# Kernel optimization log

Hardware: AMD Instinct MI355X
Metric: run time of the kernel (lower is better)

The kernel has to match this reference:

```python
import jax, jax.numpy as jnp
import numpy as np

NF = 64      # feature channels of h
K = 3        # dynamic filter spatial size (padding=1 in source implies k=3)
FACTOR = 4   # pixel-unshuffle factor


def shuffle_down(x, f):
    # torch pixel_unshuffle: (B,C,H*f,W*f) -> (B,C*f*f,H,W)
    B, C, H, W = x.shape
    x = x.reshape(B, C, H // f, f, W // f, f)
    x = x.transpose(0, 1, 3, 5, 2, 4)
    return x.reshape(B, C * f * f, H // f, W // f)


def _patches3x3(x):
    # x: (B,C,H,W) -> (B,C,9,H,W): zero-padded 3x3 neighborhoods, row-major taps,
    # identical to the identity-filter grouped conv (im2col) in the source.
    H, W = x.shape[-2], x.shape[-1]
    xp = jnp.pad(x, ((0, 0), (0, 0), (1, 1), (1, 1)))
    shifts = [xp[:, :, dy:dy + H, dx:dx + W] for dy in range(K) for dx in range(K)]
    return jnp.stack(shifts, axis=2)


def setup_inputs() -> dict:
    key = jax.random.key(0)
    k1, k2, k3, k4 = jax.random.split(key, 4)
    B, H, W = 2, 256, 256
    h = jax.random.normal(k1, (B, NF, H, W), dtype=jnp.float32)
    i_t = jax.random.normal(k2, (B, 3, H * FACTOR, W * FACTOR), dtype=jnp.float32)
    conv_w = jax.random.normal(k3, (K * K, 3 * FACTOR ** 2, K, K), dtype=jnp.float32) * 0.05
    conv_b = jax.random.normal(k4, (K * K,), dtype=jnp.float32) * 0.05
    return {"h": h, "i_t": i_t, "conv_w": conv_w, "conv_b": conv_b}


def reference(h, i_t, conv_w, conv_b):
    # predict per-pixel 3x3 filters from the shuffled-down guidance frame
    x = shuffle_down(i_t, FACTOR)  # (B, 48, H, W)
    f = jax.lax.conv_general_dilated(
        x, conv_w, window_strides=(1, 1), padding=((1, 1), (1, 1)),
        dimension_numbers=("NCHW", "OIHW", "NCHW"))
    filters = jax.nn.relu(f + conv_b[None, :, None, None])  # (B, 9, H, W)

    # dynamic per-pixel conv: same 3x3 filter applied to every channel of h
    patches = _patches3x3(h)  # (B, nf, 9, H, W)
    out = jnp.einsum("bcfhw,bfhw->bchw", patches, filters)  # (B, nf, H, W)
    return out
```

## Files before the change

### kernel.cpp

```cpp
#include <hip/hip_runtime.h>

#define HSZ 256
#define WSZ 256
#define NFC 64
#define PLANE (HSZ * WSZ)

typedef __attribute__((ext_vector_type(8))) short short8;
typedef __attribute__((ext_vector_type(4))) float f32x4;

__device__ inline unsigned short f2bf(float f) {
    unsigned u = __builtin_bit_cast(unsigned, f);
    return (unsigned short)((u + 0x7fffu + ((u >> 16) & 1u)) >> 16);
}

__global__ __launch_bounds__(256, 4) void fused_dynfilter_v4(
    const float* __restrict__ hbuf,
    const float* __restrict__ i_t,
    const float* __restrict__ wbuf,
    const float* __restrict__ bias,
    float* __restrict__ out)
{
    __shared__ __align__(16) unsigned char smem[32688];
    unsigned short* const xs  = (unsigned short*)smem;
    unsigned short* const lwT = (unsigned short*)(smem + 20160);
    float* const lf = (float*)(smem + 28080);

    const int tid = threadIdx.x;

    const int lin = blockIdx.x + 16 * (blockIdx.y + 32 * blockIdx.z);
    const int q   = ((int)gridDim.z * 512) >> 3;
    const int nid = (lin & 7) * q + (lin >> 3);
    const int b   = nid >> 9;
    const int rem = nid & 511;
    const int X0  = (rem & 15) * 16;
    const int Y0  = (rem >> 4) * 8;

    const int lane = tid & 63;
    const int l15  = lane & 15;
    const int kg   = lane >> 4;
    const int wv   = tid >> 6;

    const float bv = (l15 < 9) ? bias[l15] : 0.f;
    const float* itb = i_t + (size_t)b * 3 * (PLANE * 16);

    {
        float4 lreg[9]; int sdst[9];
#pragma unroll
        for (int k = 0; k < 9; ++k) {
            const int v = tid + 256 * k;
            const int sp = v / 12, t = v - sp * 12;
            const int c3 = t >> 2, fy = t & 3;
            const int ly = sp / 18, lx = sp - ly * 18;
            const int Y = Y0 - 1 + ly, X = X0 - 1 + lx;
            float4 val = make_float4(0.f, 0.f, 0.f, 0.f);
            if (v < 2160 && (unsigned)Y < HSZ && (unsigned)X < WSZ)
                val = *(const float4*)(itb + ((size_t)c3 * 1024 + (4 * Y + fy)) * 1024 + 4 * X);
            lreg[k] = val;
            sdst[k] = (v < 2160) ? (sp * 56 + t * 4) : -1;
        }
#pragma unroll
        for (int k = 0; k < 9; ++k)
            if (sdst[k] >= 0) {
                ushort4 u{f2bf(lreg[k].x), f2bf(lreg[k].y), f2bf(lreg[k].z), f2bf(lreg[k].w)};
                *(ushort4*)(xs + sdst[k]) = u;
            }
    }

    {
        float4 wr[4];
#pragma unroll
        for (int k = 0; k < 4; ++k) {
            const int v = tid + 256 * k;
            wr[k] = (v < 972) ? *(const float4*)(wbuf + (size_t)v * 4)
                              : make_float4(0.f, 0.f, 0.f, 0.f);
        }
#pragma unroll
        for (int k = 0; k < 4; ++k) {
            const int v = tid + 256 * k;
            if (v < 972) {
                const float e[4] = {wr[k].x, wr[k].y, wr[k].z, wr[k].w};
#pragma unroll
                for (int j = 0; j < 4; ++j) {
                    const int n  = v * 4 + j;
                    const int oc = n / 432;
                    const int r  = n - 432 * oc;
                    const int ic = r / 9;
                    const int kk = r - 9 * ic;
                    lwT[oc * 440 + kk * 48 + ic] = f2bf(e[j]);
                }
            }
        }
    }

    __syncthreads();

    short8 wf[14];
    {
        const unsigned short* lwb = lwT + l15 * 440 + kg * 8;
#pragma unroll
        for (int kb = 0; kb < 14; ++kb) {
            short8 w = {0, 0, 0, 0, 0, 0, 0, 0};
            if (l15 < 9 && !(kb == 13 && kg >= 2))
                w = *(const short8*)(lwb + kb * 32);
            wf[kb] = w;
        }
    }

    f32x4 acc0 = {0.f, 0.f, 0.f, 0.f}, acc1 = acc0;
#pragma unroll
    for (int kb = 0; kb < 14; ++kb) {
        const int k0 = kb * 32 + kg * 8;
        int off = 0;
        if (k0 < 432) {
            const int kk = k0 / 48, ic0 = k0 - 48 * kk;
            const int ky = kk / 3, kx = kk - 3 * ky;
            off = ((2 * wv + ky) * 18 + l15 + kx) * 56 + ic0;
        }
        short8 a0 = *(const short8*)(xs + off);
        short8 a1 = *(const short8*)(xs + off + 1008);
        acc0 = __builtin_amdgcn_mfma_f32_16x16x32_bf16(a0, wf[kb], acc0, 0, 0, 0);
        acc1 = __builtin_amdgcn_mfma_f32_16x16x32_bf16(a1, wf[kb], acc1, 0, 0, 0);
    }

    if (l15 < 9) {
#pragma unroll
        for (int t = 0; t < 2; ++t) {
            const int py = 2 * wv + t;
            const f32x4 A = t ? acc1 : acc0;
#pragma unroll
            for (int r = 0; r < 4; ++r)
                lf[l15 * 128 + py * 16 + (kg * 4 + r)] = fmaxf(A[r] + bv, 0.f);
        }
    }

    __syncthreads();

    const int pq  = tid & 3;
    const int pyA = (tid >> 2) & 7;
    const int clo = tid >> 5;

    float4 flt[9];
#pragma unroll
    for (int oc = 0; oc < 9; ++oc)
        flt[oc] = *(const float4*)(lf + oc * 128 + pyA * 16 + pq * 4);

    const int col0 = X0 + pq * 4;
    const int Yc   = Y0 + pyA;
    const bool gl  = (col0 > 0);
    const bool gr  = (col0 < WSZ - 4);

    bool rg[3]; int roff[3];
#pragma unroll
    for (int ky = 0; ky < 3; ++ky) {
        const int Y = Yc - 1 + ky;
        rg[ky]   = ((unsigned)Y < HSZ);
        roff[ky] = Y * WSZ + col0;
    }

    const float* hp0 = hbuf + ((size_t)b * NFC + clo) * PLANE;
    float* outp = out + ((size_t)b * NFC + clo) * PLANE + (size_t)Yc * WSZ + col0;

#pragma unroll 2
    for (int cg = 0; cg < 8; ++cg) {
        const float* p = hp0 + (size_t)cg * 8 * PLANE;

        float a[4] = {0.f, 0.f, 0.f, 0.f};
#pragma unroll
        for (int ky = 0; ky < 3; ++ky) {
            float  sl = (rg[ky] && gl) ? p[roff[ky] - 1] : 0.f;
            float4 fm = rg[ky] ? *(const float4*)(p + roff[ky])
                               : make_float4(0.f, 0.f, 0.f, 0.f);
            float  sr = (rg[ky] && gr) ? p[roff[ky] + 4] : 0.f;
            const float v6[6] = {sl, fm.x, fm.y, fm.z, fm.w, sr};
#pragma unroll
            for (int kx = 0; kx < 3; ++kx)
#pragma unroll
                for (int j = 0; j < 4; ++j)
                    a[j] = fmaf(v6[kx + j], flt[ky * 3 + kx][j], a[j]);
        }

        *(float4*)(outp + (size_t)cg * 8 * PLANE)
            = make_float4(a[0], a[1], a[2], a[3]);
    }
}

extern "C" void kernel_launch(void* const* d_in, const int* in_sizes, int n_in,
                              void* d_out, int out_size, void* d_ws, size_t ws_size,
                              hipStream_t stream) {
    const float* h      = (const float*)d_in[0];
    const float* i_t    = (const float*)d_in[1];
    const float* conv_w = (const float*)d_in[2];
    const float* conv_b = (const float*)d_in[3];
    float* out = (float*)d_out;

    const int B = in_sizes[0] / (NFC * PLANE);
    dim3 grid(WSZ / 16, HSZ / 8, B);
    fused_dynfilter_v4<<<grid, 256, 0, stream>>>(h, i_t, conv_w, conv_b, out);
}
```

Before: 130.1 us.

## Stage h halo tiles in LDS with per-wave double-buffered prefetch

```diff
diff --git a/kernel.cpp b/kernel.cpp
--- a/kernel.cpp
+++ b/kernel.cpp
@@ -13,17 +13,18 @@
     return (unsigned short)((u + 0x7fffu + ((u >> 16) & 1u)) >> 16);
 }
 
-__global__ __launch_bounds__(256, 4) void fused_dynfilter_v4(
+__global__ __launch_bounds__(256, 4) void fused_dynfilter_v5(
     const float* __restrict__ hbuf,
     const float* __restrict__ i_t,
     const float* __restrict__ wbuf,
     const float* __restrict__ bias,
     float* __restrict__ out)
 {
-    __shared__ __align__(16) unsigned char smem[32688];
+    __shared__ __align__(16) unsigned char smem[29664];
     unsigned short* const xs  = (unsigned short*)smem;
-    unsigned short* const lwT = (unsigned short*)(smem + 20160);
-    float* const lf = (float*)(smem + 28080);
+    unsigned short* const lwT = (unsigned short*)(smem + 17280);
+    float* const lf = (float*)(smem + 25056);
+    float* const hw = (float*)smem;
 
     const int tid = threadIdx.x;
 
@@ -56,7 +57,7 @@
             if (v < 2160 && (unsigned)Y < HSZ && (unsigned)X < WSZ)
                 val = *(const float4*)(itb + ((size_t)c3 * 1024 + (4 * Y + fy)) * 1024 + 4 * X);
             lreg[k] = val;
-            sdst[k] = (v < 2160) ? (sp * 56 + t * 4) : -1;
+            sdst[k] = (v < 2160) ? (sp * 48 + t * 4) : -1;
         }
 #pragma unroll
         for (int k = 0; k < 9; ++k)
@@ -86,7 +87,7 @@
                     const int r  = n - 432 * oc;
                     const int ic = r / 9;
                     const int kk = r - 9 * ic;
-                    lwT[oc * 440 + kk * 48 + ic] = f2bf(e[j]);
+                    lwT[oc * 432 + kk * 48 + ic] = f2bf(e[j]);
                 }
             }
         }
@@ -96,7 +97,7 @@
 
     short8 wf[14];
     {
-        const unsigned short* lwb = lwT + l15 * 440 + kg * 8;
+        const unsigned short* lwb = lwT + l15 * 432 + kg * 8;
 #pragma unroll
         for (int kb = 0; kb < 14; ++kb) {
             short8 w = {0, 0, 0, 0, 0, 0, 0, 0};
@@ -114,13 +115,41 @@
         if (k0 < 432) {
             const int kk = k0 / 48, ic0 = k0 - 48 * kk;
             const int ky = kk / 3, kx = kk - 3 * ky;
-            off = ((2 * wv + ky) * 18 + l15 + kx) * 56 + ic0;
+            off = ((2 * wv + ky) * 18 + l15 + kx) * 48 + ic0;
         }
         short8 a0 = *(const short8*)(xs + off);
-        short8 a1 = *(const short8*)(xs + off + 1008);
+        short8 a1 = *(const short8*)(xs + off + 864);
         acc0 = __builtin_amdgcn_mfma_f32_16x16x32_bf16(a0, wf[kb], acc0, 0, 0, 0);
         acc1 = __builtin_amdgcn_mfma_f32_16x16x32_bf16(a1, wf[kb], acc1, 0, 0, 0);
     }
+
+    const int pq  = lane & 3;
+    const int row = (lane >> 2) & 7;
+    const int c01 = lane >> 5;
+    float* const hwv = hw + wv * 1120;
+
+    auto load_h = [&](int it, float4 (&r)[2], int (&d)[2]) {
+        const float* hp0 = hbuf + ((size_t)b * NFC + wv * 16 + it * 2) * PLANE;
+#pragma unroll
+        for (int k = 0; k < 2; ++k) {
+            const int j = lane + 64 * k;
+            float4 val = make_float4(0.f, 0.f, 0.f, 0.f);
+            int dd = -1;
+            if (j < 120) {
+                const int cc  = j / 60, rr = j - 60 * cc;
+                const int rw  = rr / 6, xq = rr - 6 * rw;
+                const int Y   = Y0 - 1 + rw;
+                const int X4  = X0 - 4 + xq * 4;
+                if ((unsigned)Y < HSZ && (unsigned)X4 < WSZ)
+                    val = *(const float4*)(hp0 + (size_t)cc * PLANE + (size_t)Y * WSZ + X4);
+                dd = cc * 280 + rw * 28 + xq * 4;
+            }
+            r[k] = val; d[k] = dd;
+        }
+    };
+
+    float4 pre[2]; int pd[2];
+    load_h(0, pre, pd);
 
     if (l15 < 9) {
 #pragma unroll
@@ -135,52 +164,50 @@
 
     __syncthreads();
 
-    const int pq  = tid & 3;
-    const int pyA = (tid >> 2) & 7;
-    const int clo = tid >> 5;
-
     float4 flt[9];
 #pragma unroll
     for (int oc = 0; oc < 9; ++oc)
-        flt[oc] = *(const float4*)(lf + oc * 128 + pyA * 16 + pq * 4);
-
-    const int col0 = X0 + pq * 4;
-    const int Yc   = Y0 + pyA;
-    const bool gl  = (col0 > 0);
-    const bool gr  = (col0 < WSZ - 4);
-
-    bool rg[3]; int roff[3];
-#pragma unroll
-    for (int ky = 0; ky < 3; ++ky) {
-        const int Y = Yc - 1 + ky;
-        rg[ky]   = ((unsigned)Y < HSZ);
-        roff[ky] = Y * WSZ + col0;
-    }
-
-    const float* hp0 = hbuf + ((size_t)b * NFC + clo) * PLANE;
-    float* outp = out + ((size_t)b * NFC + clo) * PLANE + (size_t)Yc * WSZ + col0;
-
-#pragma unroll 2
-    for (int cg = 0; cg < 8; ++cg) {
-        const float* p = hp0 + (size_t)cg * 8 * PLANE;
-
+        flt[oc] = *(const float4*)(lf + oc * 128 + row * 16 + pq * 4);
+
+#pragma unroll
+    for (int k = 0; k < 2; ++k)
+        if (pd[k] >= 0) *(float4*)(hwv + pd[k]) = pre[k];
+
+    float* outp = out + ((size_t)b * NFC + wv * 16 + c01) * PLANE
+                      + (size_t)(Y0 + row) * WSZ + X0 + pq * 4;
+
+#pragma unroll
+    for (int it = 0; it < 8; ++it) {
+        const int buf = it & 1;
+
+        float4 nr[2]; int nd[2];
+        if (it < 7) load_h(it + 1, nr, nd);
+
+        const float* pl = hwv + buf * 560 + c01 * 280;
         float a[4] = {0.f, 0.f, 0.f, 0.f};
 #pragma unroll
         for (int ky = 0; ky < 3; ++ky) {
-            float  sl = (rg[ky] && gl) ? p[roff[ky] - 1] : 0.f;
-            float4 fm = rg[ky] ? *(const float4*)(p + roff[ky])
-                               : make_float4(0.f, 0.f, 0.f, 0.f);
-            float  sr = (rg[ky] && gr) ? p[roff[ky] + 4] : 0.f;
-            const float v6[6] = {sl, fm.x, fm.y, fm.z, fm.w, sr};
+            const float* rp = pl + (row + ky) * 28 + pq * 4;
+            const float4 w0 = *(const float4*)rp;
+            const float4 w1 = *(const float4*)(rp + 4);
+            const float  w8 = rp[8];
+            const float vs[9] = {w0.x, w0.y, w0.z, w0.w, w1.x, w1.y, w1.z, w1.w, w8};
 #pragma unroll
             for (int kx = 0; kx < 3; ++kx)
 #pragma unroll
                 for (int j = 0; j < 4; ++j)
-                    a[j] = fmaf(v6[kx + j], flt[ky * 3 + kx][j], a[j]);
-        }
-
-        *(float4*)(outp + (size_t)cg * 8 * PLANE)
+                    a[j] = fmaf(vs[3 + kx + j], flt[ky * 3 + kx][j], a[j]);
+        }
+
+        *(float4*)(outp + (size_t)it * 2 * PLANE)
             = make_float4(a[0], a[1], a[2], a[3]);
+
+        if (it < 7) {
+            float* hb = hwv + (buf ^ 1) * 560;
+#pragma unroll
+            for (int k = 0; k < 2; ++k)
+                if (nd[k] >= 0) *(float4*)(hb + nd[k]) = nr[k];
+        }
     }
 }
 
@@ -195,5 +222,5 @@
 
     const int B = in_sizes[0] / (NFC * PLANE);
     dim3 grid(WSZ / 16, HSZ / 8, B);
-    fused_dynfilter_v4<<<grid, 256, 0, stream>>>(h, i_t, conv_w, conv_b, out);
+    fused_dynfilter_v5<<<grid, 256, 0, stream>>>(h, i_t, conv_w, conv_b, out);
 }
```

Result: faster. 116.3 us (-10.6%).

## Widen tile to 32x8 with 512 threads and prefetch h before filter sync

Applied to the files above, without the earlier changes.

```diff
diff --git a/kernel.cpp b/kernel.cpp
--- a/kernel.cpp
+++ b/kernel.cpp
@@ -13,53 +13,55 @@
     return (unsigned short)((u + 0x7fffu + ((u >> 16) & 1u)) >> 16);
 }
 
-__global__ __launch_bounds__(256, 4) void fused_dynfilter_v4(
+__global__ __launch_bounds__(512, 4) void fused_dynfilter_v6(
     const float* __restrict__ hbuf,
     const float* __restrict__ i_t,
     const float* __restrict__ wbuf,
     const float* __restrict__ bias,
     float* __restrict__ out)
 {
-    __shared__ __align__(16) unsigned char smem[32688];
+    __shared__ __align__(16) unsigned char smem[41856];
     unsigned short* const xs  = (unsigned short*)smem;
-    unsigned short* const lwT = (unsigned short*)(smem + 20160);
-    float* const lf = (float*)(smem + 28080);
+    unsigned short* const lwT = (unsigned short*)(smem + 32640);
+    float* const lf = (float*)(smem + 32640);
 
     const int tid = threadIdx.x;
 
-    const int lin = blockIdx.x + 16 * (blockIdx.y + 32 * blockIdx.z);
-    const int q   = ((int)gridDim.z * 512) >> 3;
+    const int lin = blockIdx.x + 8 * (blockIdx.y + 32 * blockIdx.z);
+    const int q   = ((int)gridDim.z * 256) >> 3;
     const int nid = (lin & 7) * q + (lin >> 3);
-    const int b   = nid >> 9;
-    const int rem = nid & 511;
-    const int X0  = (rem & 15) * 16;
-    const int Y0  = (rem >> 4) * 8;
+    const int b   = nid >> 8;
+    const int rem = nid & 255;
+    const int X0  = (rem & 7) * 32;
+    const int Y0  = (rem >> 3) * 8;
 
     const int lane = tid & 63;
     const int l15  = lane & 15;
     const int kg   = lane >> 4;
     const int wv   = tid >> 6;
+    const int xh   = wv & 1;
+    const int r0   = (wv >> 1) * 2;
 
     const float bv = (l15 < 9) ? bias[l15] : 0.f;
     const float* itb = i_t + (size_t)b * 3 * (PLANE * 16);
 
     {
-        float4 lreg[9]; int sdst[9];
-#pragma unroll
-        for (int k = 0; k < 9; ++k) {
-            const int v = tid + 256 * k;
+        float4 lreg[8]; int sdst[8];
+#pragma unroll
+        for (int k = 0; k < 8; ++k) {
+            const int v = tid + 512 * k;
             const int sp = v / 12, t = v - sp * 12;
             const int c3 = t >> 2, fy = t & 3;
-            const int ly = sp / 18, lx = sp - ly * 18;
+            const int ly = sp / 34, lx = sp - ly * 34;
             const int Y = Y0 - 1 + ly, X = X0 - 1 + lx;
             float4 val = make_float4(0.f, 0.f, 0.f, 0.f);
-            if (v < 2160 && (unsigned)Y < HSZ && (unsigned)X < WSZ)
+            if (v < 4080 && (unsigned)Y < HSZ && (unsigned)X < WSZ)
                 val = *(const float4*)(itb + ((size_t)c3 * 1024 + (4 * Y + fy)) * 1024 + 4 * X);
             lreg[k] = val;
-            sdst[k] = (v < 2160) ? (sp * 56 + t * 4) : -1;
-        }
-#pragma unroll
-        for (int k = 0; k < 9; ++k)
+            sdst[k] = (v < 4080) ? (sp * 48 + t * 4) : -1;
+        }
+#pragma unroll
+        for (int k = 0; k < 8; ++k)
             if (sdst[k] >= 0) {
                 ushort4 u{f2bf(lreg[k].x), f2bf(lreg[k].y), f2bf(lreg[k].z), f2bf(lreg[k].w)};
                 *(ushort4*)(xs + sdst[k]) = u;
@@ -67,16 +69,16 @@
     }
 
     {
-        float4 wr[4];
-#pragma unroll
-        for (int k = 0; k < 4; ++k) {
-            const int v = tid + 256 * k;
+        float4 wr[2];
+#pragma unroll
+        for (int k = 0; k < 2; ++k) {
+            const int v = tid + 512 * k;
             wr[k] = (v < 972) ? *(const float4*)(wbuf + (size_t)v * 4)
                               : make_float4(0.f, 0.f, 0.f, 0.f);
         }
 #pragma unroll
-        for (int k = 0; k < 4; ++k) {
-            const int v = tid + 256 * k;
+        for (int k = 0; k < 2; ++k) {
+            const int v = tid + 512 * k;
             if (v < 972) {
                 const float e[4] = {wr[k].x, wr[k].y, wr[k].z, wr[k].w};
 #pragma unroll
@@ -86,7 +88,7 @@
                     const int r  = n - 432 * oc;
                     const int ic = r / 9;
                     const int kk = r - 9 * ic;
-                    lwT[oc * 440 + kk * 48 + ic] = f2bf(e[j]);
+                    lwT[oc * 432 + kk * 48 + ic] = f2bf(e[j]);
                 }
             }
         }
@@ -96,7 +98,7 @@
 
     short8 wf[14];
     {
-        const unsigned short* lwb = lwT + l15 * 440 + kg * 8;
+        const unsigned short* lwb = lwT + l15 * 432 + kg * 8;
 #pragma unroll
         for (int kb = 0; kb < 14; ++kb) {
             short8 w = {0, 0, 0, 0, 0, 0, 0, 0};
@@ -114,72 +116,93 @@
         if (k0 < 432) {
             const int kk = k0 / 48, ic0 = k0 - 48 * kk;
             const int ky = kk / 3, kx = kk - 3 * ky;
-            off = ((2 * wv + ky) * 18 + l15 + kx) * 56 + ic0;
+            off = ((r0 + ky) * 34 + 16 * xh + l15 + kx) * 48 + ic0;
         }
         short8 a0 = *(const short8*)(xs + off);
-        short8 a1 = *(const short8*)(xs + off + 1008);
+        short8 a1 = *(const short8*)(xs + off + 1632);
         acc0 = __builtin_amdgcn_mfma_f32_16x16x32_bf16(a0, wf[kb], acc0, 0, 0, 0);
         acc1 = __builtin_amdgcn_mfma_f32_16x16x32_bf16(a1, wf[kb], acc1, 0, 0, 0);
     }
 
+    __syncthreads();
+
+    const int pq  = tid & 7;
+    const int py  = (tid >> 3) & 7;
+    const int clo = tid >> 6;
+    const int col0 = X0 + pq * 4;
+    const bool gl = (col0 >= 4);
+    const bool gr = (col0 <= WSZ - 8);
+
+    bool rg[3]; int ro[3];
+#pragma unroll
+    for (int ky = 0; ky < 3; ++ky) {
+        const int Y = Y0 + py - 1 + ky;
+        rg[ky] = ((unsigned)Y < HSZ);
+        ro[ky] = Y * WSZ + col0;
+    }
+    const float* hp = hbuf + ((size_t)b * NFC + clo * 8) * PLANE;
+
+    float4 pf[9];
+#pragma unroll
+    for (int ky = 0; ky < 3; ++ky) {
+        pf[ky * 3 + 0] = (rg[ky] && gl) ? *(const float4*)(hp + ro[ky] - 4)
+                                        : make_float4(0.f, 0.f, 0.f, 0.f);
+        pf[ky * 3 + 1] = rg[ky] ? *(const float4*)(hp + ro[ky])
+                                : make_float4(0.f, 0.f, 0.f, 0.f);
+        pf[ky * 3 + 2] = (rg[ky] && gr) ? *(const float4*)(hp + ro[ky] + 4)
+                                        : make_float4(0.f, 0.f, 0.f, 0.f);
+    }
+
     if (l15 < 9) {
 #pragma unroll
         for (int t = 0; t < 2; ++t) {
-            const int py = 2 * wv + t;
+            const int pyw = r0 + t;
             const f32x4 A = t ? acc1 : acc0;
 #pragma unroll
             for (int r = 0; r < 4; ++r)
-                lf[l15 * 128 + py * 16 + (kg * 4 + r)] = fmaxf(A[r] + bv, 0.f);
+                lf[l15 * 256 + pyw * 32 + 16 * xh + kg * 4 + r] = fmaxf(A[r] + bv, 0.f);
         }
     }
 
     __syncthreads();
 
-    const int pq  = tid & 3;
-    const int pyA = (tid >> 2) & 7;
-    const int clo = tid >> 5;
-
     float4 flt[9];
 #pragma unroll
     for (int oc = 0; oc < 9; ++oc)
-        flt[oc] = *(const float4*)(lf + oc * 128 + pyA * 16 + pq * 4);
-
-    const int col0 = X0 + pq * 4;
-    const int Yc   = Y0 + pyA;
-    const bool gl  = (col0 > 0);
-    const bool gr  = (col0 < WSZ - 4);
-
-    bool rg[3]; int roff[3];
-#pragma unroll
-    for (int ky = 0; ky < 3; ++ky) {
-        const int Y = Yc - 1 + ky;
-        rg[ky]   = ((unsigned)Y < HSZ);
-        roff[ky] = Y * WSZ + col0;
-    }
-
-    const float* hp0 = hbuf + ((size_t)b * NFC + clo) * PLANE;
-    float* outp = out + ((size_t)b * NFC + clo) * PLANE + (size_t)Yc * WSZ + col0;
-
-#pragma unroll 2
-    for (int cg = 0; cg < 8; ++cg) {
-        const float* p = hp0 + (size_t)cg * 8 * PLANE;
+        flt[oc] = *(const float4*)(lf + oc * 256 + py * 32 + pq * 4);
+
+    float* op = out + ((size_t)b * NFC + clo * 8) * PLANE
+                    + (size_t)(Y0 + py) * WSZ + col0;
+
+#pragma unroll
+    for (int it = 0; it < 8; ++it) {
+        const float* p = hp + (size_t)it * PLANE;
 
         float a[4] = {0.f, 0.f, 0.f, 0.f};
 #pragma unroll
         for (int ky = 0; ky < 3; ++ky) {
-            float  sl = (rg[ky] && gl) ? p[roff[ky] - 1] : 0.f;
-            float4 fm = rg[ky] ? *(const float4*)(p + roff[ky])
-                               : make_float4(0.f, 0.f, 0.f, 0.f);
-            float  sr = (rg[ky] && gr) ? p[roff[ky] + 4] : 0.f;
-            const float v6[6] = {sl, fm.x, fm.y, fm.z, fm.w, sr};
+            float4 lv, mv, rv;
+            if (it == 0) {
+                lv = pf[ky * 3 + 0]; mv = pf[ky * 3 + 1]; rv = pf[ky * 3 + 2];
+            } else {
+                lv = (rg[ky] && gl) ? *(const float4*)(p + ro[ky] - 4)
+                                    : make_float4(0.f, 0.f, 0.f, 0.f);
+                mv = rg[ky] ? *(const float4*)(p + ro[ky])
+                            : make_float4(0.f, 0.f, 0.f, 0.f);
+                rv = (rg[ky] && gr) ? *(const float4*)(p + ro[ky] + 4)
+                                    : make_float4(0.f, 0.f, 0.f, 0.f);
+            }
+            const float vs[12] = {lv.x, lv.y, lv.z, lv.w,
+                                  mv.x, mv.y, mv.z, mv.w,
+                                  rv.x, rv.y, rv.z, rv.w};
 #pragma unroll
             for (int kx = 0; kx < 3; ++kx)
 #pragma unroll
                 for (int j = 0; j < 4; ++j)
-                    a[j] = fmaf(v6[kx + j], flt[ky * 3 + kx][j], a[j]);
-        }
-
-        *(float4*)(outp + (size_t)cg * 8 * PLANE)
+                    a[j] = fmaf(vs[3 + kx + j], flt[ky * 3 + kx][j], a[j]);
+        }
+
+        *(float4*)(op + (size_t)it * PLANE)
             = make_float4(a[0], a[1], a[2], a[3]);
     }
 }
@@ -194,6 +217,6 @@
     float* out = (float*)d_out;
 
     const int B = in_sizes[0] / (NFC * PLANE);
-    dim3 grid(WSZ / 16, HSZ / 8, B);
-    fused_dynfilter_v4<<<grid, 256, 0, stream>>>(h, i_t, conv_w, conv_b, out);
+    dim3 grid(8, 32, B);
+    fused_dynfilter_v6<<<grid, 512, 0, stream>>>(h, i_t, conv_w, conv_b, out);
 }
```

New measurement: 120.1 us. 1.08x faster.
